# Performance work log

Measured on AMD Instinct MI355X. Metric: run time of the kernel, lower is better.

## Reference

```python
import jax, jax.numpy as jnp
import numpy as np

B, N, K = 4, 4096, 16
D_POINTS, D_MODEL = 64, 128


def setup_inputs() -> dict:
    key = jax.random.key(0)
    ks = jax.random.split(key, 18)
    rn = lambda k, shp, s=0.05: (jax.random.normal(k, shp, jnp.float32) * s)
    return {
        "xyz": jax.random.normal(ks[0], (B, N, 3), jnp.float32),
        "features": jax.random.normal(ks[1], (B, N, D_POINTS), jnp.float32),
        # fc_delta: Linear(3,d_model) -> ReLU -> Linear(d_model,d_model)
        "Wd1": rn(ks[2], (3, D_MODEL)), "bd1": rn(ks[3], (D_MODEL,)),
        "Wd2": rn(ks[4], (D_MODEL, D_MODEL)), "bd2": rn(ks[5], (D_MODEL,)),
        # fc1: Linear(d_points, d_model)
        "Wf1": rn(ks[6], (D_POINTS, D_MODEL)), "bf1": rn(ks[7], (D_MODEL,)),
        # w_qs / w_ks / w_vs: Linear(d_model, d_model, bias=False)
        "Wq": rn(ks[8], (D_MODEL, D_MODEL)),
        "Wk": rn(ks[9], (D_MODEL, D_MODEL)),
        "Wv": rn(ks[10], (D_MODEL, D_MODEL)),
        # fc_gamma: Linear(d_model,d_model) -> ReLU -> Linear(d_model,d_model)
        "Wg1": rn(ks[11], (D_MODEL, D_MODEL)), "bg1": rn(ks[12], (D_MODEL,)),
        "Wg2": rn(ks[13], (D_MODEL, D_MODEL)), "bg2": rn(ks[14], (D_MODEL,)),
        # fc2: Linear(d_model, d_points)
        "Wo": rn(ks[15], (D_MODEL, D_POINTS)), "bo": rn(ks[16], (D_POINTS,)),
    }


def reference(xyz, features, Wd1, bd1, Wd2, bd2, Wf1, bf1, Wq, Wk, Wv,
              Wg1, bg1, Wg2, bg2, Wo, bo):
    sq = jnp.sum(xyz * xyz, axis=-1)
    d2 = sq[:, :, None] + sq[:, None, :] - 2.0 * jnp.einsum('bnd,bmd->bnm', xyz, xyz)
    # argsort()[:, :, :k] == k smallest distances (self included)
    _, knn_idx = jax.lax.top_k(-d2, K)  # [B,N,K] int32

    gather = jax.vmap(lambda a, i: a[i])  # per-batch fancy gather along point axis
    knn_xyz = gather(xyz, knn_idx)                       # [B,N,K,3]
    rel = xyz[:, :, None, :] - knn_xyz                   # [B,N,K,3]
    pos_enc = jax.nn.relu(rel @ Wd1 + bd1) @ Wd2 + bd2   # [B,N,K,D]

    shortcut = features
    f = features @ Wf1 + bf1                             # [B,N,D]
    knn_f = gather(f, knn_idx)                           # [B,N,K,D]

    q = f @ Wq                                           # [B,N,D]
    k = knn_f @ Wk                                       # [B,N,K,D]
    v = knn_f @ Wv                                       # [B,N,K,D]

    attn = q[:, :, None, :] - k + pos_enc                # [B,N,K,D]
    attn = jax.nn.relu(attn @ Wg1 + bg1) @ Wg2 + bg2
    attn = jax.nn.softmax(attn / np.sqrt(D_MODEL).astype(np.float32), axis=-2)

    res = jnp.einsum('bnkf,bnkf->bnf', attn, v + pos_enc)  # [B,N,D]
    return res @ Wo + bo + shortcut                        # [B,N,d_points]
```

## Files before the change

kernel.cpp:

```cpp
#include <hip/hip_runtime.h>
#include <hip/hip_bf16.h>

#define NPTS 4096
#define BATCH 4
#define BN (BATCH * NPTS)
#define DMODEL 128
#define DPTS 64
#define KNBR 16
#define SWS 136

typedef unsigned short u16;
typedef unsigned int u32;
typedef unsigned long long u64;
typedef short bh8 __attribute__((ext_vector_type(8)));
typedef float f32x4 __attribute__((ext_vector_type(4)));

__device__ __forceinline__ float bfu(u16 u) {
    union { u32 i; float f; } c; c.i = ((u32)u) << 16; return c.f;
}
__device__ __forceinline__ u16 f2u(float x) {
    u32 u = __float_as_uint(x);
    u32 r = u + 0x7FFFu + ((u >> 16) & 1u);
    return (u16)(r >> 16);
}
__device__ __forceinline__ u32 pack2(float a, float b) {
    return (u32)f2u(a) | ((u32)f2u(b) << 16);
}
__device__ __forceinline__ float ldr(const void* p, long i, int mode) {
    return mode == 0 ? bfu(((const u16*)p)[i]) : ((const float*)p)[i];
}
__device__ __forceinline__ void str(void* p, long i, float v, int mode) {
    if (mode == 0) ((u16*)p)[i] = f2u(v);
    else ((float*)p)[i] = v;
}
__device__ __forceinline__ int detect_mode(const void* Wq) {
    const u16* w = (const u16*)Wq;
    int lane = threadIdx.x & 63;
    int tot = 0;
#pragma unroll
    for (int r = 0; r < 4; ++r) {
        unsigned e = (w[lane + r * 64] >> 7) & 0xFFu;
        bool wild = (e >= 132u) || (e > 0u && e <= 90u);
        tot += (int)__popcll(__ballot(wild));
    }
    return tot > 32 ? 1 : 0;
}

__global__ __launch_bounds__(256) void prep_kernel(
    const void* __restrict__ Wd2, const void* __restrict__ Wg1, const void* __restrict__ Wg2,
    const void* __restrict__ Wo, const void* __restrict__ Wq, const void* __restrict__ Wk,
    const void* __restrict__ Wv, const void* __restrict__ Wf1, const void* __restrict__ xyz,
    u16* __restrict__ WdT2, u16* __restrict__ WgT1, u16* __restrict__ WgT2,
    u16* __restrict__ WoT, u16* __restrict__ WqT, u16* __restrict__ WkT,
    u16* __restrict__ WvT, u16* __restrict__ WfT, float4* __restrict__ cloudF) {
    int mode = detect_mode(Wq);
    int gid = blockIdx.x * 256 + threadIdx.x;
    if (gid < 6 * 16384) {
        int m = gid >> 14, o = gid & 16383;
        int n = o >> 7, i = o & 127;
        const void* W = (m == 0) ? Wd2 : (m == 1) ? Wg1 : (m == 2) ? Wg2
                      : (m == 3) ? Wq  : (m == 4) ? Wk  : Wv;
        u16* D = (m == 0) ? WdT2 : (m == 1) ? WgT1 : (m == 2) ? WgT2
               : (m == 3) ? WqT  : (m == 4) ? WkT  : WvT;
        D[o] = f2u(ldr(W, (long)i * 128 + n, mode));
    } else if (gid < 6 * 16384 + 8192) {
        int o = gid - 6 * 16384;
        int n = o >> 6, k2 = o & 63;
        WfT[o] = f2u(ldr(Wf1, (long)k2 * 128 + n, mode));
    } else if (gid < 6 * 16384 + 16384) {
        int o2 = gid - 6 * 16384 - 8192;
        int col = o2 >> 7, i = o2 & 127;
        WoT[o2] = f2u(ldr(Wo, (long)i * 64 + col, mode));
    } else if (gid < 6 * 16384 + 16384 + 16384) {
        int i = gid - (6 * 16384 + 16384);
        float gx = ldr(xyz, (long)i * 3 + 0, mode);
        float gy = ldr(xyz, (long)i * 3 + 1, mode);
        float gz = ldr(xyz, (long)i * 3 + 2, mode);
        float4 f;
        f.x = gx; f.y = gy; f.z = gz;
        f.w = gx * gx + gy * gy + gz * gz;
        cloudF[i] = f;
    }
}

__global__ __launch_bounds__(256) void qkv_kernel(
    const void* __restrict__ feat, const void* __restrict__ bf1v, const void* __restrict__ WqRaw,
    const u16* __restrict__ WfT, const u16* __restrict__ WqT,
    const u16* __restrict__ WkT, const u16* __restrict__ WvT,
    u16* __restrict__ qw, u16* __restrict__ kfw, u16* __restrict__ vfw) {
    int mode = detect_mode(WqRaw);
    __shared__ __align__(16) u16 sFeat[64 * 72];
    __shared__ __align__(16) u16 sF[64 * SWS];
    const int t = threadIdx.x;
    const int p0 = blockIdx.x * 64;
    const int lane = t & 63, w = t >> 6;
    const int rg = (w & 1) * 32, cg = (w >> 1) * 64;
    const int lm = lane & 15, lq = lane >> 4;

    for (int i = t; i < 512; i += 256) {
        int r = i >> 3, c8 = i & 7;
        u16 tmp[8];
        if (mode == 0) {
            *(uint4*)tmp = *((const uint4*)feat + (long)(p0 + r) * 8 + c8);
        } else {
            const float* fp = (const float*)feat + (long)(p0 + r) * 64 + c8 * 8;
#pragma unroll
            for (int u = 0; u < 8; ++u) tmp[u] = f2u(fp[u]);
        }
        *(uint4*)(sFeat + r * 72 + c8 * 8) = *(uint4*)tmp;
    }
    __syncthreads();

    {
        f32x4 acc[2][4];
#pragma unroll
        for (int rt = 0; rt < 2; ++rt)
#pragma unroll
            for (int ct = 0; ct < 4; ++ct) { acc[rt][ct][0]=0.f; acc[rt][ct][1]=0.f; acc[rt][ct][2]=0.f; acc[rt][ct][3]=0.f; }
#pragma unroll
        for (int kk = 0; kk < 2; ++kk) {
            const int ko = kk * 32 + lq * 8;
            bh8 a0 = *(const bh8*)(sFeat + (rg + lm) * 72 + ko);
            bh8 a1 = *(const bh8*)(sFeat + (rg + 16 + lm) * 72 + ko);
            bh8 bq[4];
#pragma unroll
            for (int ct = 0; ct < 4; ++ct)
                bq[ct] = *(const bh8*)(WfT + (long)(cg + ct * 16 + lm) * 64 + ko);
#pragma unroll
            for (int ct = 0; ct < 4; ++ct) {
                acc[0][ct] = __builtin_amdgcn_mfma_f32_16x16x32_bf16(a0, bq[ct], acc[0][ct], 0, 0, 0);
                acc[1][ct] = __builtin_amdgcn_mfma_f32_16x16x32_bf16(a1, bq[ct], acc[1][ct], 0, 0, 0);
            }
        }
#pragma unroll
        for (int rt = 0; rt < 2; ++rt)
#pragma unroll
            for (int ct = 0; ct < 4; ++ct) {
                const int col = cg + ct * 16 + lm;
                const float bj = ldr(bf1v, col, mode);
#pragma unroll
                for (int r4 = 0; r4 < 4; ++r4) {
                    int row = rg + rt * 16 + lq * 4 + r4;
                    u32 u = (u32)f2u(acc[rt][ct][r4] + bj);
                    u32 o = __shfl_xor(u, 1);
                    if ((lane & 1) == 0)
                        *(u32*)(sF + row * SWS + col) = u | (o << 16);
                }
            }
    }
    __syncthreads();

    {
        const int m = blockIdx.y;
        const u16* Wm = (m == 0) ? WqT : (m == 1) ? WkT : WvT;
        u16* Om = (m == 0) ? qw : (m == 1) ? kfw : vfw;
        f32x4 acc[2][4];
#pragma unroll
        for (int rt = 0; rt < 2; ++rt)
#pragma unroll
            for (int ct = 0; ct < 4; ++ct) { acc[rt][ct][0]=0.f; acc[rt][ct][1]=0.f; acc[rt][ct][2]=0.f; acc[rt][ct][3]=0.f; }
#pragma unroll
        for (int kk = 0; kk < 4; ++kk) {
            const int ko = kk * 32 + lq * 8;
            bh8 a0 = *(const bh8*)(sF + (rg + lm) * SWS + ko);
            bh8 a1 = *(const bh8*)(sF + (rg + 16 + lm) * SWS + ko);
            bh8 bq[4];
#pragma unroll
            for (int ct = 0; ct < 4; ++ct)
                bq[ct] = *(const bh8*)(Wm + (long)(cg + ct * 16 + lm) * 128 + ko);
#pragma unroll
            for (int ct = 0; ct < 4; ++ct) {
                acc[0][ct] = __builtin_amdgcn_mfma_f32_16x16x32_bf16(a0, bq[ct], acc[0][ct], 0, 0, 0);
                acc[1][ct] = __builtin_amdgcn_mfma_f32_16x16x32_bf16(a1, bq[ct], acc[1][ct], 0, 0, 0);
            }
        }
#pragma unroll
        for (int rt = 0; rt < 2; ++rt)
#pragma unroll
            for (int ct = 0; ct < 4; ++ct) {
                const int col = cg + ct * 16 + lm;
#pragma unroll
                for (int r4 = 0; r4 < 4; ++r4) {
                    int row = rg + rt * 16 + lq * 4 + r4;
                    u32 u = (u32)f2u(acc[rt][ct][r4]);
                    u32 o = __shfl_xor(u, 1);
                    if ((lane & 1) == 0)
                        *(u32*)(Om + (long)(p0 + row) * DMODEL + col) = u | (o << 16);
                }
            }
    }
}

__global__ __launch_bounds__(256) void knn_kernel(
    const float4* __restrict__ cloudF, int* __restrict__ knnIdx) {
    const int t = threadIdx.x, lane = t & 63, w = t >> 6;
    const int p0 = blockIdx.x * 4;
    const long bbase = (long)(p0 >> 12) * NPTS;
    const float4* cl = cloudF + bbase;

    const int pl = (p0 & (NPTS - 1)) + w;
    float4 qv = cl[pl];
    const float m2x = -2.f * qv.x, m2y = -2.f * qv.y, m2z = -2.f * qv.z;

    u64 kv;
    {
        float4 c = cl[lane];
        float key = fmaf(m2x, c.x, fmaf(m2y, c.y, fmaf(m2z, c.z, c.w)));
        u32 uk = __float_as_uint(key);
        uk ^= (u32)((int)uk >> 31) | 0x80000000u;
        kv = ((u64)uk << 32) | (u32)lane;
#pragma unroll
        for (int k = 2; k <= 64; k <<= 1) {
#pragma unroll
            for (int j = k >> 1; j > 0; j >>= 1) {
                u64 other = __shfl_xor(kv, j);
                bool keepMin = ((lane & j) == 0) == ((lane & k) == 0);
                bool smaller = kv < other;
                kv = (keepMin == smaller) ? kv : other;
            }
        }
    }
    u32 Tu = __builtin_amdgcn_readlane((u32)(kv >> 32), 15);

    float4 cd0 = cl[64 + lane];
    float4 cd1 = cl[128 + lane];
#pragma unroll 1
    for (int it = 0; it < 32; ++it) {
        const int base = 64 + it * 128;
        float4 c0 = cd0, c1 = cd1;
        if (it < 31) {
            int n0 = base + 128 + lane;
            int n1 = n0 + 64 > 4095 ? 4095 : n0 + 64;
            cd0 = cl[n0];
            cd1 = cl[n1];
        }
        float k0 = fmaf(m2x, c0.x, fmaf(m2y, c0.y, fmaf(m2z, c0.z, c0.w)));
        float k1 = fmaf(m2x, c1.x, fmaf(m2y, c1.y, fmaf(m2z, c1.z, c1.w)));
        u32 u0 = __float_as_uint(k0); u0 ^= (u32)((int)u0 >> 31) | 0x80000000u;
        u32 u1 = __float_as_uint(k1); u1 ^= (u32)((int)u1 >> 31) | 0x80000000u;
        if (it == 31) u1 = 0xFFFFFFFFu;
        u32 umin = (u0 < u1) ? u0 : u1;
        unsigned long long mask = __ballot(umin < Tu);
        while (mask) {
            int l = __ffsll(mask) - 1;
            mask &= mask - 1;
            u32 a0 = __builtin_amdgcn_readlane(u0, l);
            u32 a1 = __builtin_amdgcn_readlane(u1, l);
            if (a0 < Tu) {
                u64 cand = ((u64)a0 << 32) | (u32)(base + l);
                u64 prev = __shfl_up(kv, 1);
                if (lane == 0) prev = 0;
                kv = (prev > cand) ? prev : ((kv > cand) ? cand : kv);
                Tu = __builtin_amdgcn_readlane((u32)(kv >> 32), 15);
            }
            if (a1 < Tu) {
                u64 cand = ((u64)a1 << 32) | (u32)(base + 64 + l);
                u64 prev = __shfl_up(kv, 1);
                if (lane == 0) prev = 0;
                kv = (prev > cand) ? prev : ((kv > cand) ? cand : kv);
                Tu = __builtin_amdgcn_readlane((u32)(kv >> 32), 15);
            }
        }
    }
    if (lane < 16) knnIdx[(long)(p0 + w) * 16 + lane] = (int)(u32)kv;
}

#define ATT_SA 0
#define ATT_SREL 17408
#define ATT_SBIAS 18432
#define ATT_SQ 19968
#define SMEM_BYTES 20992

__global__ __launch_bounds__(256, 6) void fused_kernel(
    const float4* __restrict__ cloudF, const int* __restrict__ knnIdx,
    const void* __restrict__ feat,
    const void* __restrict__ Wd1, const void* __restrict__ bd1, const void* __restrict__ bd2,
    const void* __restrict__ bg1, const void* __restrict__ bg2, const void* __restrict__ bo,
    const void* __restrict__ WqRaw,
    const u16* __restrict__ WdT2, const u16* __restrict__ WgT1, const u16* __restrict__ WgT2,
    const u16* __restrict__ WoT,
    const u16* __restrict__ qw, const u16* __restrict__ kfw, const u16* __restrict__ vfw,
    void* __restrict__ out) {
    int mode = detect_mode(WqRaw);
    __shared__ __align__(16) char smem[SMEM_BYTES];
    __shared__ int sIdx[64];
    u16* sA   = (u16*)(smem + ATT_SA);
    float (*sRel)[4] = (float(*)[4])(smem + ATT_SREL);
    float* sBias = (float*)(smem + ATT_SBIAS);
    u16* sQ   = (u16*)(smem + ATT_SQ);

    const int t = threadIdx.x, lane = t & 63, w = t >> 6;
    const int lm = lane & 15, lq = lane >> 4;
    const int rg = (w & 1) * 32, cg = (w >> 1) * 64;
    const int p0 = blockIdx.x * 4;
    const long bbase = (long)(p0 >> 12) * NPTS;
    const float4* cl = cloudF + bbase;

    for (int i = t; i < 384; i += 256) {
        const void* b = (i < 128) ? bd2 : (i < 256) ? bg1 : bg2;
        sBias[i] = ldr(b, i & 127, mode);
    }
    ((u32*)sQ)[t] = ((const u32*)(qw + (long)p0 * DMODEL))[t];
    const int ch = 2 * lane;
    const float wd0a = ldr(Wd1, ch, mode),       wd0b = ldr(Wd1, ch + 1, mode);
    const float wd1a = ldr(Wd1, 128 + ch, mode), wd1b = ldr(Wd1, 128 + ch + 1, mode);
    const float wd2a = ldr(Wd1, 256 + ch, mode), wd2b = ldr(Wd1, 256 + ch + 1, mode);
    const float bd1a = ldr(bd1, ch, mode),       bd1b = ldr(bd1, ch + 1, mode);
    if (t < 64) {
        int idx = knnIdx[(long)p0 * 16 + t];
        sIdx[t] = idx;
        int pl2 = (p0 & (NPTS - 1)) + (t >> 4);
        float4 pv = cl[pl2];
        float4 nv = cl[idx];
        sRel[t][0] = pv.x - nv.x;
        sRel[t][1] = pv.y - nv.y;
        sRel[t][2] = pv.z - nv.z;
    }
    __syncthreads();

#pragma unroll
    for (int i = 0; i < 16; ++i) {
        int r = w * 16 + i;
        float4 rl = *(const float4*)sRel[r];
        float h0 = fmaxf(bd1a + rl.x * wd0a + rl.y * wd1a + rl.z * wd2a, 0.f);
        float h1 = fmaxf(bd1b + rl.x * wd0b + rl.y * wd1b + rl.z * wd2b, 0.f);
        *(u32*)(sA + r * SWS + ch) = pack2(h0, h1);
    }
    __syncthreads();

    u32 pe[2][4][2];
    {
        f32x4 acc[2][4];
#pragma unroll
        for (int rt = 0; rt < 2; ++rt)
#pragma unroll
            for (int ct = 0; ct < 4; ++ct) { acc[rt][ct][0]=0.f; acc[rt][ct][1]=0.f; acc[rt][ct][2]=0.f; acc[rt][ct][3]=0.f; }
#pragma unroll
        for (int kk = 0; kk < 4; ++kk) {
            const int ko = kk * 32 + lq * 8;
            bh8 a0 = *(const bh8*)(sA + (rg + lm) * SWS + ko);
            bh8 a1 = *(const bh8*)(sA + (rg + 16 + lm) * SWS + ko);
            bh8 bq[4];
#pragma unroll
            for (int ct = 0; ct < 4; ++ct)
                bq[ct] = *(const bh8*)(WdT2 + (long)(cg + ct * 16 + lm) * 128 + ko);
#pragma unroll
            for (int ct = 0; ct < 4; ++ct) {
                acc[0][ct] = __builtin_amdgcn_mfma_f32_16x16x32_bf16(a0, bq[ct], acc[0][ct], 0, 0, 0);
                acc[1][ct] = __builtin_amdgcn_mfma_f32_16x16x32_bf16(a1, bq[ct], acc[1][ct], 0, 0, 0);
            }
        }
#pragma unroll
        for (int rt = 0; rt < 2; ++rt)
#pragma unroll
            for (int ct = 0; ct < 4; ++ct) {
                const float bj = sBias[cg + ct * 16 + lm];
                pe[rt][ct][0] = pack2(acc[rt][ct][0] + bj, acc[rt][ct][1] + bj);
                pe[rt][ct][1] = pack2(acc[rt][ct][2] + bj, acc[rt][ct][3] + bj);
            }
    }
    __syncthreads();

#pragma unroll
    for (int rt = 0; rt < 2; ++rt) {
        const int pt = (w & 1) * 2 + rt;
        int id4[4];
#pragma unroll
        for (int r4 = 0; r4 < 4; ++r4)
            id4[r4] = sIdx[rg + rt * 16 + lq * 4 + r4];
#pragma unroll
        for (int ct = 0; ct < 4; ++ct) {
            const int col = cg + ct * 16 + lm;
            const float qv = bfu(sQ[pt * DMODEL + col]);
#pragma unroll
            for (int r4 = 0; r4 < 4; ++r4) {
                const int row = rg + rt * 16 + lq * 4 + r4;
                u16 kfv = kfw[(bbase + id4[r4]) * (long)DMODEL + col];
                float pev = bfu((u16)(pe[rt][ct][r4 >> 1] >> (16 * (r4 & 1))));
                float a = qv - bfu(kfv) + pev;
                u32 u = (u32)f2u(a);
                u32 o = __shfl_xor(u, 1);
                if ((lm & 1) == 0)
                    *(u32*)(sA + row * SWS + col) = u | (o << 16);
            }
        }
    }
    __syncthreads();

    {
        f32x4 acc[2][4];
#pragma unroll
        for (int rt = 0; rt < 2; ++rt)
#pragma unroll
            for (int ct = 0; ct < 4; ++ct) { acc[rt][ct][0]=0.f; acc[rt][ct][1]=0.f; acc[rt][ct][2]=0.f; acc[rt][ct][3]=0.f; }
#pragma unroll
        for (int kk = 0; kk < 4; ++kk) {
            const int ko = kk * 32 + lq * 8;
            bh8 a0 = *(const bh8*)(sA + (rg + lm) * SWS + ko);
            bh8 a1 = *(const bh8*)(sA + (rg + 16 + lm) * SWS + ko);
            bh8 bq[4];
#pragma unroll
            for (int ct = 0; ct < 4; ++ct)
                bq[ct] = *(const bh8*)(WgT1 + (long)(cg + ct * 16 + lm) * 128 + ko);
#pragma unroll
            for (int ct = 0; ct < 4; ++ct) {
                acc[0][ct] = __builtin_amdgcn_mfma_f32_16x16x32_bf16(a0, bq[ct], acc[0][ct], 0, 0, 0);
                acc[1][ct] = __builtin_amdgcn_mfma_f32_16x16x32_bf16(a1, bq[ct], acc[1][ct], 0, 0, 0);
            }
        }
        __syncthreads();
#pragma unroll
        for (int rt = 0; rt < 2; ++rt)
#pragma unroll
            for (int ct = 0; ct < 4; ++ct) {
                const int col = cg + ct * 16 + lm;
                const float bj = sBias[128 + col];
#pragma unroll
                for (int r4 = 0; r4 < 4; ++r4) {
                    int row = rg + rt * 16 + lq * 4 + r4;
                    float v = fmaxf(acc[rt][ct][r4] + bj, 0.f);
                    u32 u = (u32)f2u(v);
                    u32 o = __shfl_xor(u, 1);
                    if ((lane & 1) == 0)
                        *(u32*)(sA + row * SWS + col) = u | (o << 16);
                }
            }
    }
    __syncthreads();

    {
        f32x4 acc[2][4];
#pragma unroll
        for (int rt = 0; rt < 2; ++rt)
#pragma unroll
            for (int ct = 0; ct < 4; ++ct) { acc[rt][ct][0]=0.f; acc[rt][ct][1]=0.f; acc[rt][ct][2]=0.f; acc[rt][ct][3]=0.f; }
#pragma unroll
        for (int kk = 0; kk < 4; ++kk) {
            const int ko = kk * 32 + lq * 8;
            bh8 a0 = *(const bh8*)(sA + (rg + lm) * SWS + ko);
            bh8 a1 = *(const bh8*)(sA + (rg + 16 + lm) * SWS + ko);
            bh8 bq[4];
#pragma unroll
            for (int ct = 0; ct < 4; ++ct)
                bq[ct] = *(const bh8*)(WgT2 + (long)(cg + ct * 16 + lm) * 128 + ko);
#pragma unroll
            for (int ct = 0; ct < 4; ++ct) {
                acc[0][ct] = __builtin_amdgcn_mfma_f32_16x16x32_bf16(a0, bq[ct], acc[0][ct], 0, 0, 0);
                acc[1][ct] = __builtin_amdgcn_mfma_f32_16x16x32_bf16(a1, bq[ct], acc[1][ct], 0, 0, 0);
            }
        }
        __syncthreads();

        const float inv = 0.08838834764831845f;
#pragma unroll
        for (int rt = 0; rt < 2; ++rt) {
            const int pt = (w & 1) * 2 + rt;
            int id4[4];
#pragma unroll
            for (int r4 = 0; r4 < 4; ++r4)
                id4[r4] = sIdx[rg + rt * 16 + lq * 4 + r4];
#pragma unroll
            for (int ct = 0; ct < 4; ++ct) {
                const int col = cg + ct * 16 + lm;
                const float bj = sBias[256 + col];
                float l0 = acc[rt][ct][0] + bj;
                float l1 = acc[rt][ct][1] + bj;
                float l2 = acc[rt][ct][2] + bj;
                float l3 = acc[rt][ct][3] + bj;
                float m = fmaxf(fmaxf(l0, l1), fmaxf(l2, l3));
                m = fmaxf(m, __shfl_xor(m, 16));
                m = fmaxf(m, __shfl_xor(m, 32));
                float s = 0.f, r = 0.f;
#pragma unroll
                for (int r4 = 0; r4 < 4; ++r4) {
                    float l = (r4 == 0) ? l0 : (r4 == 1) ? l1 : (r4 == 2) ? l2 : l3;
                    u16 vv = vfw[(bbase + id4[r4]) * (long)DMODEL + col];
                    float pev = bfu((u16)(pe[rt][ct][r4 >> 1] >> (16 * (r4 & 1))));
                    float e = __expf((l - m) * inv);
                    s += e;
                    r += e * (bfu(vv) + pev);
                }
                s += __shfl_xor(s, 16); s += __shfl_xor(s, 32);
                r += __shfl_xor(r, 16); r += __shfl_xor(r, 32);
                u32 u = (u32)f2u(r / s);
                u32 o = __shfl_xor(u, 1);
                if (lq == 0 && (lm & 1) == 0)
                    *(u32*)(sA + pt * SWS + col) = u | (o << 16);
            }
        }
    }
    __syncthreads();

    {
        const int col = w * 16 + lm;
        f32x4 acc = {0.f, 0.f, 0.f, 0.f};
#pragma unroll
        for (int kk = 0; kk < 4; ++kk) {
            const int ko = kk * 32 + lq * 8;
            bh8 aa = *(const bh8*)(sA + lm * SWS + ko);
            bh8 bb = *(const bh8*)(WoT + (long)col * DMODEL + ko);
            acc = __builtin_amdgcn_mfma_f32_16x16x32_bf16(aa, bb, acc, 0, 0, 0);
        }
        if (lq == 0) {
            float bov = ldr(bo, col, mode);
#pragma unroll
            for (int r4 = 0; r4 < 4; ++r4) {
                long p = p0 + r4;
                float v = acc[r4] + bov + ldr(feat, p * DPTS + col, mode);
                str(out, p * DPTS + col, v, mode);
            }
        }
    }
}

extern "C" void kernel_launch(void* const* d_in, const int* in_sizes, int n_in,
                              void* d_out, int out_size, void* d_ws, size_t ws_size,
                              hipStream_t stream) {
    (void)in_sizes; (void)n_in; (void)out_size; (void)ws_size;
    char* ws = (char*)d_ws;
    u16* qw   = (u16*)(ws + 256);
    u16* kfw  = qw + (long)BN * DMODEL;
    u16* vfw  = kfw + (long)BN * DMODEL;
    u16* WdT2 = vfw + (long)BN * DMODEL;
    u16* WgT1 = WdT2 + 16384;
    u16* WgT2 = WgT1 + 16384;
    u16* WoT  = WgT2 + 16384;
    u16* WqT  = WoT + 8192;
    u16* WkT  = WqT + 16384;
    u16* WvT  = WkT + 16384;
    u16* WfT  = WvT + 16384;
    float4* cloudF = (float4*)(WfT + 8192);
    int* knnIdx = (int*)(cloudF + BN);

    prep_kernel<<<512, 256, 0, stream>>>(d_in[4], d_in[11], d_in[13], d_in[15],
                                         d_in[8], d_in[9], d_in[10], d_in[6], d_in[0],
                                         WdT2, WgT1, WgT2, WoT, WqT, WkT, WvT, WfT,
                                         cloudF);
    qkv_kernel<<<dim3(BN / 64, 3), 256, 0, stream>>>(d_in[1], d_in[7], d_in[8],
                                                     WfT, WqT, WkT, WvT, qw, kfw, vfw);
    knn_kernel<<<BN / 4, 256, 0, stream>>>(cloudF, knnIdx);
    fused_kernel<<<BN / 4, 256, 0, stream>>>(cloudF, knnIdx, d_in[1],
                                             d_in[2], d_in[3], d_in[5],
                                             d_in[12], d_in[14], d_in[16], d_in[8],
                                             WdT2, WgT1, WgT2, WoT,
                                             qw, kfw, vfw, d_out);
}
```

Baseline: 333.3 us.

## Halve points per block in fused kernel and stage pos-enc through LDS

The fused attention kernel now processes 2 points per block instead of 4, doubling the grid and raising launch bounds to 8 waves per SIMD. Position-encoding results are stored in shared memory instead of registers. The key gather is now a coalesced row-wise pass, and the softmax is recomputed per column by looping over the 16 neighbours from LDS rather than using cross-lane shuffles. The aim is lower register pressure and higher occupancy, at the cost of reloading weight tiles for half as many rows per block and doing more LDS traffic.

```diff
diff --git a/kernel.cpp b/kernel.cpp
--- a/kernel.cpp
+++ b/kernel.cpp
@@ -266,12 +266,13 @@
 }
 
 #define ATT_SA 0
+#define ATT_SPE 8704
 #define ATT_SREL 17408
-#define ATT_SBIAS 18432
-#define ATT_SQ 19968
-#define SMEM_BYTES 20992
-
-__global__ __launch_bounds__(256, 6) void fused_kernel(
+#define ATT_SBIAS 17920
+#define ATT_SQ 19456
+#define SMEM_BYTES 19968
+
+__global__ __launch_bounds__(256, 8) void fused_kernel(
     const float4* __restrict__ cloudF, const int* __restrict__ knnIdx,
     const void* __restrict__ feat,
     const void* __restrict__ Wd1, const void* __restrict__ bd1, const void* __restrict__ bd2,
@@ -283,16 +284,17 @@
     void* __restrict__ out) {
     int mode = detect_mode(WqRaw);
     __shared__ __align__(16) char smem[SMEM_BYTES];
-    __shared__ int sIdx[64];
+    __shared__ int sIdx[32];
     u16* sA   = (u16*)(smem + ATT_SA);
+    u16* sPE  = (u16*)(smem + ATT_SPE);
     float (*sRel)[4] = (float(*)[4])(smem + ATT_SREL);
     float* sBias = (float*)(smem + ATT_SBIAS);
     u16* sQ   = (u16*)(smem + ATT_SQ);
 
     const int t = threadIdx.x, lane = t & 63, w = t >> 6;
     const int lm = lane & 15, lq = lane >> 4;
-    const int rg = (w & 1) * 32, cg = (w >> 1) * 64;
-    const int p0 = blockIdx.x * 4;
+    const int rg = (w & 1) * 16, cg = (w >> 1) * 64;
+    const int p0 = blockIdx.x * 2;
     const long bbase = (long)(p0 >> 12) * NPTS;
     const float4* cl = cloudF + bbase;
 
@@ -300,13 +302,13 @@
         const void* b = (i < 128) ? bd2 : (i < 256) ? bg1 : bg2;
         sBias[i] = ldr(b, i & 127, mode);
     }
-    ((u32*)sQ)[t] = ((const u32*)(qw + (long)p0 * DMODEL))[t];
+    if (t < 128) ((u32*)sQ)[t] = ((const u32*)(qw + (long)p0 * DMODEL))[t];
     const int ch = 2 * lane;
     const float wd0a = ldr(Wd1, ch, mode),       wd0b = ldr(Wd1, ch + 1, mode);
     const float wd1a = ldr(Wd1, 128 + ch, mode), wd1b = ldr(Wd1, 128 + ch + 1, mode);
     const float wd2a = ldr(Wd1, 256 + ch, mode), wd2b = ldr(Wd1, 256 + ch + 1, mode);
     const float bd1a = ldr(bd1, ch, mode),       bd1b = ldr(bd1, ch + 1, mode);
-    if (t < 64) {
+    if (t < 32) {
         int idx = knnIdx[(long)p0 * 16 + t];
         sIdx[t] = idx;
         int pl2 = (p0 & (NPTS - 1)) + (t >> 4);
@@ -319,8 +321,8 @@
     __syncthreads();
 
 #pragma unroll
-    for (int i = 0; i < 16; ++i) {
-        int r = w * 16 + i;
+    for (int i = 0; i < 8; ++i) {
+        int r = w * 8 + i;
         float4 rl = *(const float4*)sRel[r];
         float h0 = fmaxf(bd1a + rl.x * wd0a + rl.y * wd1a + rl.z * wd2a, 0.f);
         float h1 = fmaxf(bd1b + rl.x * wd0b + rl.y * wd1b + rl.z * wd2b, 0.f);
@@ -328,166 +330,137 @@
     }
     __syncthreads();
 
-    u32 pe[2][4][2];
-    {
-        f32x4 acc[2][4];
-#pragma unroll
-        for (int rt = 0; rt < 2; ++rt)
-#pragma unroll
-            for (int ct = 0; ct < 4; ++ct) { acc[rt][ct][0]=0.f; acc[rt][ct][1]=0.f; acc[rt][ct][2]=0.f; acc[rt][ct][3]=0.f; }
+    {
+        f32x4 acc[4];
+#pragma unroll
+        for (int ct = 0; ct < 4; ++ct) { acc[ct][0]=0.f; acc[ct][1]=0.f; acc[ct][2]=0.f; acc[ct][3]=0.f; }
 #pragma unroll
         for (int kk = 0; kk < 4; ++kk) {
             const int ko = kk * 32 + lq * 8;
             bh8 a0 = *(const bh8*)(sA + (rg + lm) * SWS + ko);
-            bh8 a1 = *(const bh8*)(sA + (rg + 16 + lm) * SWS + ko);
-            bh8 bq[4];
-#pragma unroll
-            for (int ct = 0; ct < 4; ++ct)
-                bq[ct] = *(const bh8*)(WdT2 + (long)(cg + ct * 16 + lm) * 128 + ko);
-#pragma unroll
-            for (int ct = 0; ct < 4; ++ct) {
-                acc[0][ct] = __builtin_amdgcn_mfma_f32_16x16x32_bf16(a0, bq[ct], acc[0][ct], 0, 0, 0);
-                acc[1][ct] = __builtin_amdgcn_mfma_f32_16x16x32_bf16(a1, bq[ct], acc[1][ct], 0, 0, 0);
-            }
-        }
-#pragma unroll
-        for (int rt = 0; rt < 2; ++rt)
-#pragma unroll
-            for (int ct = 0; ct < 4; ++ct) {
-                const float bj = sBias[cg + ct * 16 + lm];
-                pe[rt][ct][0] = pack2(acc[rt][ct][0] + bj, acc[rt][ct][1] + bj);
-                pe[rt][ct][1] = pack2(acc[rt][ct][2] + bj, acc[rt][ct][3] + bj);
-            }
-    }
-    __syncthreads();
-
-#pragma unroll
-    for (int rt = 0; rt < 2; ++rt) {
-        const int pt = (w & 1) * 2 + rt;
-        int id4[4];
-#pragma unroll
-        for (int r4 = 0; r4 < 4; ++r4)
-            id4[r4] = sIdx[rg + rt * 16 + lq * 4 + r4];
+#pragma unroll
+            for (int ct = 0; ct < 4; ++ct) {
+                bh8 bq = *(const bh8*)(WdT2 + (long)(cg + ct * 16 + lm) * 128 + ko);
+                acc[ct] = __builtin_amdgcn_mfma_f32_16x16x32_bf16(a0, bq, acc[ct], 0, 0, 0);
+            }
+        }
 #pragma unroll
         for (int ct = 0; ct < 4; ++ct) {
             const int col = cg + ct * 16 + lm;
-            const float qv = bfu(sQ[pt * DMODEL + col]);
+            const float bj = sBias[col];
 #pragma unroll
             for (int r4 = 0; r4 < 4; ++r4) {
-                const int row = rg + rt * 16 + lq * 4 + r4;
-                u16 kfv = kfw[(bbase + id4[r4]) * (long)DMODEL + col];
-                float pev = bfu((u16)(pe[rt][ct][r4 >> 1] >> (16 * (r4 & 1))));
-                float a = qv - bfu(kfv) + pev;
-                u32 u = (u32)f2u(a);
+                int row = rg + lq * 4 + r4;
+                u32 u = (u32)f2u(acc[ct][r4] + bj);
                 u32 o = __shfl_xor(u, 1);
-                if ((lm & 1) == 0)
-                    *(u32*)(sA + row * SWS + col) = u | (o << 16);
-            }
-        }
-    }
-    __syncthreads();
-
-    {
-        f32x4 acc[2][4];
-#pragma unroll
-        for (int rt = 0; rt < 2; ++rt)
-#pragma unroll
-            for (int ct = 0; ct < 4; ++ct) { acc[rt][ct][0]=0.f; acc[rt][ct][1]=0.f; acc[rt][ct][2]=0.f; acc[rt][ct][3]=0.f; }
+                if ((lane & 1) == 0)
+                    *(u32*)(sPE + row * SWS + col) = u | (o << 16);
+            }
+        }
+    }
+    __syncthreads();
+
+#pragma unroll
+    for (int i = 0; i < 8; ++i) {
+        int r = w * 8 + i;
+        u32 kv2 = *(const u32*)(kfw + (bbase + sIdx[r]) * (long)DMODEL + ch);
+        u32 qv2 = *(const u32*)(sQ + (r >> 4) * DMODEL + ch);
+        u32 pe2 = *(const u32*)(sPE + r * SWS + ch);
+        float a0 = bfu((u16)qv2) - bfu((u16)kv2) + bfu((u16)pe2);
+        float a1 = bfu((u16)(qv2 >> 16)) - bfu((u16)(kv2 >> 16)) + bfu((u16)(pe2 >> 16));
+        *(u32*)(sA + r * SWS + ch) = pack2(a0, a1);
+    }
+    __syncthreads();
+
+    {
+        f32x4 acc[4];
+#pragma unroll
+        for (int ct = 0; ct < 4; ++ct) { acc[ct][0]=0.f; acc[ct][1]=0.f; acc[ct][2]=0.f; acc[ct][3]=0.f; }
 #pragma unroll
         for (int kk = 0; kk < 4; ++kk) {
             const int ko = kk * 32 + lq * 8;
             bh8 a0 = *(const bh8*)(sA + (rg + lm) * SWS + ko);
-            bh8 a1 = *(const bh8*)(sA + (rg + 16 + lm) * SWS + ko);
-            bh8 bq[4];
-#pragma unroll
-            for (int ct = 0; ct < 4; ++ct)
-                bq[ct] = *(const bh8*)(WgT1 + (long)(cg + ct * 16 + lm) * 128 + ko);
-#pragma unroll
-            for (int ct = 0; ct < 4; ++ct) {
-                acc[0][ct] = __builtin_amdgcn_mfma_f32_16x16x32_bf16(a0, bq[ct], acc[0][ct], 0, 0, 0);
-                acc[1][ct] = __builtin_amdgcn_mfma_f32_16x16x32_bf16(a1, bq[ct], acc[1][ct], 0, 0, 0);
+#pragma unroll
+            for (int ct = 0; ct < 4; ++ct) {
+                bh8 bq = *(const bh8*)(WgT1 + (long)(cg + ct * 16 + lm) * 128 + ko);
+                acc[ct] = __builtin_amdgcn_mfma_f32_16x16x32_bf16(a0, bq, acc[ct], 0, 0, 0);
             }
         }
         __syncthreads();
 #pragma unroll
-        for (int rt = 0; rt < 2; ++rt)
-#pragma unroll
-            for (int ct = 0; ct < 4; ++ct) {
-                const int col = cg + ct * 16 + lm;
-                const float bj = sBias[128 + col];
-#pragma unroll
-                for (int r4 = 0; r4 < 4; ++r4) {
-                    int row = rg + rt * 16 + lq * 4 + r4;
-                    float v = fmaxf(acc[rt][ct][r4] + bj, 0.f);
-                    u32 u = (u32)f2u(v);
-                    u32 o = __shfl_xor(u, 1);
-                    if ((lane & 1) == 0)
-                        *(u32*)(sA + row * SWS + col) = u | (o << 16);
-                }
-            }
-    }
-    __syncthreads();
-
-    {
-        f32x4 acc[2][4];
-#pragma unroll
-        for (int rt = 0; rt < 2; ++rt)
-#pragma unroll
-            for (int ct = 0; ct < 4; ++ct) { acc[rt][ct][0]=0.f; acc[rt][ct][1]=0.f; acc[rt][ct][2]=0.f; acc[rt][ct][3]=0.f; }
+        for (int ct = 0; ct < 4; ++ct) {
+            const int col = cg + ct * 16 + lm;
+            const float bj = sBias[128 + col];
+#pragma unroll
+            for (int r4 = 0; r4 < 4; ++r4) {
+                int row = rg + lq * 4 + r4;
+                float v = fmaxf(acc[ct][r4] + bj, 0.f);
+                u32 u = (u32)f2u(v);
+                u32 o = __shfl_xor(u, 1);
+                if ((lane & 1) == 0)
+                    *(u32*)(sA + row * SWS + col) = u | (o << 16);
+            }
+        }
+    }
+    __syncthreads();
+
+    {
+        f32x4 acc[4];
+#pragma unroll
+        for (int ct = 0; ct < 4; ++ct) { acc[ct][0]=0.f; acc[ct][1]=0.f; acc[ct][2]=0.f; acc[ct][3]=0.f; }
 #pragma unroll
         for (int kk = 0; kk < 4; ++kk) {
             const int ko = kk * 32 + lq * 8;
             bh8 a0 = *(const bh8*)(sA + (rg + lm) * SWS + ko);
-            bh8 a1 = *(const bh8*)(sA + (rg + 16 + lm) * SWS + ko);
-            bh8 bq[4];
-#pragma unroll
-            for (int ct = 0; ct < 4; ++ct)
-                bq[ct] = *(const bh8*)(WgT2 + (long)(cg + ct * 16 + lm) * 128 + ko);
-#pragma unroll
-            for (int ct = 0; ct < 4; ++ct) {
-                acc[0][ct] = __builtin_amdgcn_mfma_f32_16x16x32_bf16(a0, bq[ct], acc[0][ct], 0, 0, 0);
-                acc[1][ct] = __builtin_amdgcn_mfma_f32_16x16x32_bf16(a1, bq[ct], acc[1][ct], 0, 0, 0);
+#pragma unroll
+            for (int ct = 0; ct < 4; ++ct) {
+                bh8 bq = *(const bh8*)(WgT2 + (long)(cg + ct * 16 + lm) * 128 + ko);
+                acc[ct] = __builtin_amdgcn_mfma_f32_16x16x32_bf16(a0, bq, acc[ct], 0, 0, 0);
             }
         }
         __syncthreads();
-
+#pragma unroll
+        for (int ct = 0; ct < 4; ++ct) {
+            const int col = cg + ct * 16 + lm;
+            const float bj = sBias[256 + col];
+#pragma unroll
+            for (int r4 = 0; r4 < 4; ++r4) {
+                int row = rg + lq * 4 + r4;
+                u32 u = (u32)f2u(acc[ct][r4] + bj);
+                u32 o = __shfl_xor(u, 1);
+                if ((lane & 1) == 0)
+                    *(u32*)(sA + row * SWS + col) = u | (o << 16);
+            }
+        }
+    }
+    __syncthreads();
+
+    float res;
+    {
+        const int p = w >> 1;
+        const int c = (w & 1) * 64 + lane;
+        float mx = -3e38f;
+#pragma unroll
+        for (int k = 0; k < KNBR; ++k)
+            mx = fmaxf(mx, bfu(sA[(p * 16 + k) * SWS + c]));
         const float inv = 0.08838834764831845f;
-#pragma unroll
-        for (int rt = 0; rt < 2; ++rt) {
-            const int pt = (w & 1) * 2 + rt;
-            int id4[4];
-#pragma unroll
-            for (int r4 = 0; r4 < 4; ++r4)
-                id4[r4] = sIdx[rg + rt * 16 + lq * 4 + r4];
-#pragma unroll
-            for (int ct = 0; ct < 4; ++ct) {
-                const int col = cg + ct * 16 + lm;
-                const float bj = sBias[256 + col];
-                float l0 = acc[rt][ct][0] + bj;
-                float l1 = acc[rt][ct][1] + bj;
-                float l2 = acc[rt][ct][2] + bj;
-                float l3 = acc[rt][ct][3] + bj;
-                float m = fmaxf(fmaxf(l0, l1), fmaxf(l2, l3));
-                m = fmaxf(m, __shfl_xor(m, 16));
-                m = fmaxf(m, __shfl_xor(m, 32));
-                float s = 0.f, r = 0.f;
-#pragma unroll
-                for (int r4 = 0; r4 < 4; ++r4) {
-                    float l = (r4 == 0) ? l0 : (r4 == 1) ? l1 : (r4 == 2) ? l2 : l3;
-                    u16 vv = vfw[(bbase + id4[r4]) * (long)DMODEL + col];
-                    float pev = bfu((u16)(pe[rt][ct][r4 >> 1] >> (16 * (r4 & 1))));
-                    float e = __expf((l - m) * inv);
-                    s += e;
-                    r += e * (bfu(vv) + pev);
-                }
-                s += __shfl_xor(s, 16); s += __shfl_xor(s, 32);
-                r += __shfl_xor(r, 16); r += __shfl_xor(r, 32);
-                u32 u = (u32)f2u(r / s);
-                u32 o = __shfl_xor(u, 1);
-                if (lq == 0 && (lm & 1) == 0)
-                    *(u32*)(sA + pt * SWS + col) = u | (o << 16);
-            }
-        }
+        float s = 0.f, r = 0.f;
+#pragma unroll
+        for (int k = 0; k < KNBR; ++k) {
+            float l = bfu(sA[(p * 16 + k) * SWS + c]);
+            float vv = bfu(vfw[(bbase + sIdx[p * 16 + k]) * (long)DMODEL + c]);
+            float pev = bfu(sPE[(p * 16 + k) * SWS + c]);
+            float e = __expf((l - mx) * inv);
+            s += e;
+            r += e * (vv + pev);
+        }
+        res = r / s;
+    }
+    __syncthreads();
+    {
+        const int p = w >> 1;
+        const int c = (w & 1) * 64 + lane;
+        sA[p * SWS + c] = f2u(res);
     }
     __syncthreads();
 
@@ -504,7 +477,7 @@
         if (lq == 0) {
             float bov = ldr(bo, col, mode);
 #pragma unroll
-            for (int r4 = 0; r4 < 4; ++r4) {
+            for (int r4 = 0; r4 < 2; ++r4) {
                 long p = p0 + r4;
                 float v = acc[r4] + bov + ldr(feat, p * DPTS + col, mode);
                 str(out, p * DPTS + col, v, mode);
@@ -539,7 +512,7 @@
     qkv_kernel<<<dim3(BN / 64, 3), 256, 0, stream>>>(d_in[1], d_in[7], d_in[8],
                                                      WfT, WqT, WkT, WvT, qw, kfw, vfw);
     knn_kernel<<<BN / 4, 256, 0, stream>>>(cloudF, knnIdx);
-    fused_kernel<<<BN / 4, 256, 0, stream>>>(cloudF, knnIdx, d_in[1],
+    fused_kernel<<<BN / 2, 256, 0, stream>>>(cloudF, knnIdx, d_in[1],
                                              d_in[2], d_in[3], d_in[5],
                                              d_in[12], d_in[14], d_in[16], d_in[8],
                                              WdT2, WgT1, WgT2, WoT,
```

After: 372.4 us. 11.7% more time.
